# Kernel optimization log

Hardware: AMD Instinct MI355X
Metric: run time of the kernel (lower is better)

## Reference

```python
import jax, jax.numpy as jnp
import numpy as np

B, P, N, C = 8, 4, 512, 768
H = 12
HD = C // H  # 64
SCALE = HD ** -0.5


def setup_inputs() -> dict:
    key = jax.random.key(0)
    k1, k2, k3 = jax.random.split(key, 3)
    x = jax.random.normal(k1, (B, P, N, C), dtype=jnp.float32)
    W_qkv = jax.random.normal(k2, (3 * C, C), dtype=jnp.float32) * (C ** -0.5)
    W_proj = jax.random.normal(k3, (C, C), dtype=jnp.float32) * (C ** -0.5)
    b_proj = jnp.zeros((C,), dtype=jnp.float32)
    return {"x": x, "W_qkv": W_qkv, "W_proj": W_proj, "b_proj": b_proj}


def reference(x, W_qkv, W_proj, b_proj):
    b, p, n, c = x.shape
    # qkv projection (no bias): (B,P,N,3C) -> (B,P,N,3,H,HD)
    qkv = jnp.einsum('bpnc,dc->bpnd', x, W_qkv).reshape(b, p, n, 3, H, HD)
    # -> (3, B, P, H, N, HD)
    qkv = jnp.transpose(qkv, (3, 0, 1, 4, 2, 5))
    q, k, v = qkv[0], qkv[1], qkv[2]
    # scaled dot-product attention per (batch, patch, head)
    attn = jnp.einsum('bphnd,bphmd->bphnm', q * SCALE, k)
    attn = jax.nn.softmax(attn, axis=-1)
    out = jnp.einsum('bphnm,bphmd->bphnd', attn, v)
    # merge heads: (B,P,N,H,HD) -> (B,P,N,C)
    out = jnp.transpose(out, (0, 1, 3, 2, 4)).reshape(b, p, n, c)
    return jnp.einsum('bpnc,dc->bpnd', out, W_proj) + b_proj
```

## Files before the change

### kernel.cpp

```cpp
#include <hip/hip_runtime.h>

typedef _Float16 f16x8 __attribute__((ext_vector_type(8)));
typedef _Float16 f16x4 __attribute__((ext_vector_type(4)));
typedef unsigned short u16x8 __attribute__((ext_vector_type(8)));
typedef unsigned short u16x4 __attribute__((ext_vector_type(4)));
typedef float f32x4 __attribute__((ext_vector_type(4)));

#define GLOAD_LDS16(GP, LP)                                                        \
  __builtin_amdgcn_global_load_lds((const __attribute__((address_space(1))) void*)(GP), \
                                   (__attribute__((address_space(3))) void*)(LP), 16, 0, 0)

__device__ __forceinline__ unsigned int pkh(float a, float b) {
  return __builtin_bit_cast(unsigned int, __builtin_amdgcn_cvt_pkrtz(a, b));
}
__device__ __forceinline__ f16x8 ldfragh(const unsigned short* p) {
  return __builtin_bit_cast(f16x8, *(const u16x8*)p);
}
__device__ __forceinline__ f16x4 ldfragh4(const unsigned short* p) {
  return __builtin_bit_cast(f16x4, *(const u16x4*)p);
}
__device__ __forceinline__ f32x4 mfma32h(f16x8 a, f16x8 b, f32x4 c) {
  return __builtin_amdgcn_mfma_f32_16x16x32_f16(a, b, c, 0, 0, 0);
}
__device__ __forceinline__ f32x4 mfma16h(f16x4 a, f16x4 b, f32x4 c) {
  return __builtin_amdgcn_mfma_f32_16x16x16f16(a, b, c, 0, 0, 0);
}

#define MTOK   16384
#define CDIM   768
#define C3     2304
#define C2     1536
#define NX     12582912
#define NQW    1769472
#define NPW    589824

#define QSCALE_LOG2E 0.1803368801111204f

#define XB_OFF    0ul
#define WQKV_OFF  25165824ul
#define WPROJ_OFF 28704768ul
#define QK_OFF    29884416ul
#define VT_OFF    80216064ul

__global__ __launch_bounds__(256) void convert_kernel(
    const float* __restrict__ x, const float* __restrict__ wqkv,
    const float* __restrict__ wproj, unsigned short* __restrict__ xb,
    unsigned short* __restrict__ wqkvb, unsigned short* __restrict__ wprojb) {
  const int NX4 = NX / 4, NQ4 = NQW / 4, NP4 = NPW / 4;
  const int total = NX4 + NQ4 + NP4;
  for (int i = blockIdx.x * 256 + threadIdx.x; i < total; i += gridDim.x * 256) {
    const float4* src; unsigned short* dst; float scale = 1.f; int j;
    if (i < NX4) { src = (const float4*)x; dst = xb; j = i; }
    else if (i < NX4 + NQ4) {
      j = i - NX4; src = (const float4*)wqkv; dst = wqkvb;
      int d = (j * 4) / CDIM; if (d < CDIM) scale = QSCALE_LOG2E;
    } else { j = i - NX4 - NQ4; src = (const float4*)wproj; dst = wprojb; }
    float4 v = src[j];
    uint2 pk; pk.x = pkh(v.x * scale, v.y * scale); pk.y = pkh(v.z * scale, v.w * scale);
    *(uint2*)(dst + (long)j * 4) = pk;
  }
}

template <int MODE>
__global__ __launch_bounds__(256) void gemm_bt(
    const unsigned short* __restrict__ A, const unsigned short* __restrict__ B,
    unsigned short* __restrict__ out_hf, float* __restrict__ out_f32,
    const float* __restrict__ bias) {
  constexpr int K = 768;
  constexpr bool SWAP = (MODE != 1);
  __shared__ unsigned short As[128 * 64];
  __shared__ unsigned short Bs[128 * 64];
  const int tid = threadIdx.x;
  const int wave = tid >> 6, lane = tid & 63;
  const int wy = wave >> 1, wx = wave & 1;
  const int l15 = lane & 15, quad = lane >> 4;
  const int bm = blockIdx.x, bn = blockIdx.y;

  f32x4 acc[4][4];
  for (int i = 0; i < 4; i++)
    for (int j = 0; j < 4; j++) acc[i][j] = f32x4{0.f, 0.f, 0.f, 0.f};

  const long Abase = (long)bm * 128 * K;
  const long Bbase = (long)bn * 128 * K;

  long goff[4]; int ldsoff[4];
  for (int i = 0; i < 4; i++) {
    int c = wave * 256 + i * 64 + lane;
    int row = c >> 3, q = c & 7;
    int srcq = q ^ (row & 7);
    goff[i] = (long)row * K + srcq * 8;
    ldsoff[i] = c * 8;
  }
  const int slot0 = (quad ^ (l15 & 7)) * 8;
  const int slot1 = ((4 + quad) ^ (l15 & 7)) * 8;

  for (int kk = 0; kk < K; kk += 64) {
    for (int i = 0; i < 4; i++) {
      GLOAD_LDS16(A + Abase + goff[i] + kk, As + ldsoff[i]);
      GLOAD_LDS16(B + Bbase + goff[i] + kk, Bs + ldsoff[i]);
    }
    __syncthreads();
    for (int ks = 0; ks < 2; ks++) {
      const int sl = ks ? slot1 : slot0;
      f16x8 af[4], bfr[4];
      for (int mt = 0; mt < 4; mt++) af[mt]  = ldfragh(As + (wy * 64 + mt * 16 + l15) * 64 + sl);
      for (int nt = 0; nt < 4; nt++) bfr[nt] = ldfragh(Bs + (wx * 64 + nt * 16 + l15) * 64 + sl);
      for (int mt = 0; mt < 4; mt++)
        for (int nt = 0; nt < 4; nt++) {
          if (SWAP) acc[mt][nt] = mfma32h(bfr[nt], af[mt], acc[mt][nt]);
          else      acc[mt][nt] = mfma32h(af[mt], bfr[nt], acc[mt][nt]);
        }
    }
    __syncthreads();
  }

  if (MODE == 0) {
    for (int mt = 0; mt < 4; mt++) {
      int m = bm * 128 + wy * 64 + mt * 16 + l15;
      for (int nt = 0; nt < 4; nt++) {
        int d0 = bn * 128 + wx * 64 + nt * 16 + quad * 4;
        uint2 pk; pk.x = pkh(acc[mt][nt][0], acc[mt][nt][1]);
        pk.y = pkh(acc[mt][nt][2], acc[mt][nt][3]);
        *(uint2*)(out_hf + (long)m * C2 + d0) = pk;
      }
    }
  } else if (MODE == 1) {
    for (int mt = 0; mt < 4; mt++) {
      int mg = bm * 128 + wy * 64 + mt * 16 + quad * 4;
      int bp = mg >> 9, n0 = mg & 511;
      for (int nt = 0; nt < 4; nt++) {
        int dp = bn * 128 + wx * 64 + nt * 16 + l15;
        int hh = dp >> 6, e = dp & 63;
        uint2 pk; pk.x = pkh(acc[mt][nt][0], acc[mt][nt][1]);
        pk.y = pkh(acc[mt][nt][2], acc[mt][nt][3]);
        *(uint2*)(out_hf + ((long)((bp * 12 + hh) * 64 + e) * 512 + n0)) = pk;
      }
    }
  } else {
    for (int nt = 0; nt < 4; nt++) {
      int d0 = bn * 128 + wx * 64 + nt * 16 + quad * 4;
      float4 bv = *(const float4*)(bias + d0);
      for (int mt = 0; mt < 4; mt++) {
        int m = bm * 128 + wy * 64 + mt * 16 + l15;
        float4 o;
        o.x = acc[mt][nt][0] + bv.x; o.y = acc[mt][nt][1] + bv.y;
        o.z = acc[mt][nt][2] + bv.z; o.w = acc[mt][nt][3] + bv.w;
        *(float4*)(out_f32 + (long)m * CDIM + d0) = o;
      }
    }
  }
}

__global__ __launch_bounds__(256, 4) void attn_kernel(
    const unsigned short* __restrict__ qk, const unsigned short* __restrict__ vT,
    unsigned short* __restrict__ aout) {
  const int bph = blockIdx.x;
  const int qt  = blockIdx.y;
  const int bp = bph / 12, h = bph % 12;
  const int tid = threadIdx.x;
  const int wave = tid >> 6, lane = tid & 63;
  const int l15 = lane & 15, quad = lane >> 4;

  __shared__ unsigned short Qs[128 * 72];
  __shared__ unsigned short Ks[64 * 72];
  __shared__ unsigned short Vs[64 * 72];

  const unsigned short* Qg = qk + (long)(bp * 512 + qt * 128) * C2 + h * 64;
  const unsigned short* Kg = qk + (long)(bp * 512) * C2 + CDIM + h * 64;
  const unsigned short* Vg = vT + (long)(bp * 12 + h) * 64 * 512;

  for (int i = 0; i < 4; i++) {
    int c = tid + i * 256;
    int row = c >> 3, c8 = c & 7;
    *(uint4*)(Qs + row * 72 + c8 * 8) = *(const uint4*)(Qg + (long)row * C2 + c8 * 8);
  }

  f32x4 o[2][4];
  float lrow[2] = {0.f, 0.f};
  for (int a = 0; a < 2; a++)
    for (int b = 0; b < 4; b++) o[a][b] = f32x4{0.f, 0.f, 0.f, 0.f};

  for (int ch = 0; ch < 8; ch++) {
    if (ch) __syncthreads();
    for (int i = 0; i < 2; i++) {
      int c = tid + i * 256;
      int row = c >> 3, c8 = c & 7;
      *(uint4*)(Ks + row * 72 + c8 * 8) = *(const uint4*)(Kg + (long)(ch * 64 + row) * C2 + c8 * 8);
      *(uint4*)(Vs + row * 72 + c8 * 8) = *(const uint4*)(Vg + (long)row * 512 + ch * 64 + c8 * 8);
    }
    __syncthreads();

    f32x4 st[2][4];
    for (int a = 0; a < 2; a++)
      for (int b = 0; b < 4; b++) st[a][b] = f32x4{0.f, 0.f, 0.f, 0.f};
    for (int ks = 0; ks < 2; ks++) {
      f16x8 qf[2];
      qf[0] = ldfragh(Qs + (wave * 32 +      l15) * 72 + ks * 32 + quad * 8);
      qf[1] = ldfragh(Qs + (wave * 32 + 16 + l15) * 72 + ks * 32 + quad * 8);
      for (int nt = 0; nt < 4; nt++) {
        f16x8 kf = ldfragh(Ks + (nt * 16 + l15) * 72 + ks * 32 + quad * 8);
        st[0][nt] = mfma32h(kf, qf[0], st[0][nt]);
        st[1][nt] = mfma32h(kf, qf[1], st[1][nt]);
      }
    }

    f16x4 pf[2][4];
    for (int mt2 = 0; mt2 < 2; mt2++) {
      float rs = 0.f;
      for (int nt = 0; nt < 4; nt++) {
        f32x4 p;
        for (int r = 0; r < 4; r++) {
          p[r] = __builtin_amdgcn_exp2f(st[mt2][nt][r]);
          rs += p[r];
        }
        uint2 pk2; pk2.x = pkh(p[0], p[1]); pk2.y = pkh(p[2], p[3]);
        pf[mt2][nt] = __builtin_bit_cast(f16x4, pk2);
      }
      lrow[mt2] += rs;
    }

    for (int nt = 0; nt < 4; nt++)
      for (int et = 0; et < 4; et++) {
        f16x4 vf = ldfragh4(Vs + (et * 16 + l15) * 72 + nt * 16 + quad * 4);
        o[0][et] = mfma16h(vf, pf[0][nt], o[0][et]);
        o[1][et] = mfma16h(vf, pf[1][nt], o[1][et]);
      }
  }

  for (int mt2 = 0; mt2 < 2; mt2++) {
    float l = lrow[mt2];
    l += __shfl_xor(l, 16);
    l += __shfl_xor(l, 32);
    float inv = 1.f / l;
    int q = qt * 128 + wave * 32 + mt2 * 16 + l15;
    for (int et = 0; et < 4; et++) {
      uint2 pk; pk.x = pkh(o[mt2][et][0] * inv, o[mt2][et][1] * inv);
      pk.y = pkh(o[mt2][et][2] * inv, o[mt2][et][3] * inv);
      *(uint2*)(aout + (long)(bp * 512 + q) * CDIM + h * 64 + et * 16 + quad * 4) = pk;
    }
  }
}

extern "C" void kernel_launch(void* const* d_in, const int* in_sizes, int n_in,
                              void* d_out, int out_size, void* d_ws, size_t ws_size,
                              hipStream_t stream) {
  (void)in_sizes; (void)n_in; (void)out_size; (void)ws_size;
  const float* x     = (const float*)d_in[0];
  const float* wqkv  = (const float*)d_in[1];
  const float* wproj = (const float*)d_in[2];
  const float* bproj = (const float*)d_in[3];
  float* out = (float*)d_out;
  char* ws = (char*)d_ws;

  unsigned short* xb     = (unsigned short*)(ws + XB_OFF);
  unsigned short* wqkvb  = (unsigned short*)(ws + WQKV_OFF);
  unsigned short* wprojb = (unsigned short*)(ws + WPROJ_OFF);
  unsigned short* qkbuf  = (unsigned short*)(ws + QK_OFF);
  unsigned short* vTbuf  = (unsigned short*)(ws + VT_OFF);
  unsigned short* attn_o = xb;

  convert_kernel<<<2048, 256, 0, stream>>>(x, wqkv, wproj, xb, wqkvb, wprojb);
  gemm_bt<0><<<dim3(128, 12), 256, 0, stream>>>(xb, wqkvb, qkbuf, nullptr, nullptr);
  gemm_bt<1><<<dim3(128, 6), 256, 0, stream>>>(xb, wqkvb + (long)C2 * CDIM, vTbuf, nullptr, nullptr);
  attn_kernel<<<dim3(384, 4), 256, 0, stream>>>(qkbuf, vTbuf, attn_o);
  gemm_bt<2><<<dim3(128, 6), 256, 0, stream>>>(attn_o, wprojb, nullptr, out, bproj);
}
```

Before: 262.3 us.

## Merge QK and V projection GEMMs and register-prefetch tiles instead of LDS-direct loads

The separate QK and V projection launches become one launch over an 18-column grid. Blocks with bn<12 write the row-major QK buffer, and the rest write the transposed V buffer, using a runtime swap flag to pick the MFMA operand order. The direct global-to-LDS loads are replaced by a register prefetch: the next K-slice is loaded into registers while MFMAs run on the current LDS tile. This removes one launch and its tail and overlaps global latency with compute, but costs more registers, adds an extra store pass through VGPRs, and makes the MFMA operand order a runtime branch.

```diff
diff --git a/kernel.cpp b/kernel.cpp
--- a/kernel.cpp
+++ b/kernel.cpp
@@ -5,10 +5,6 @@
 typedef unsigned short u16x8 __attribute__((ext_vector_type(8)));
 typedef unsigned short u16x4 __attribute__((ext_vector_type(4)));
 typedef float f32x4 __attribute__((ext_vector_type(4)));
-
-#define GLOAD_LDS16(GP, LP)                                                        \
-  __builtin_amdgcn_global_load_lds((const __attribute__((address_space(1))) void*)(GP), \
-                                   (__attribute__((address_space(3))) void*)(LP), 16, 0, 0)
 
 __device__ __forceinline__ unsigned int pkh(float a, float b) {
   return __builtin_bit_cast(unsigned int, __builtin_amdgcn_cvt_pkrtz(a, b));
@@ -64,10 +60,9 @@
 template <int MODE>
 __global__ __launch_bounds__(256) void gemm_bt(
     const unsigned short* __restrict__ A, const unsigned short* __restrict__ B,
-    unsigned short* __restrict__ out_hf, float* __restrict__ out_f32,
-    const float* __restrict__ bias) {
+    unsigned short* __restrict__ out_hf, unsigned short* __restrict__ out_vT,
+    float* __restrict__ out_f32, const float* __restrict__ bias) {
   constexpr int K = 768;
-  constexpr bool SWAP = (MODE != 1);
   __shared__ unsigned short As[128 * 64];
   __shared__ unsigned short Bs[128 * 64];
   const int tid = threadIdx.x;
@@ -75,13 +70,14 @@
   const int wy = wave >> 1, wx = wave & 1;
   const int l15 = lane & 15, quad = lane >> 4;
   const int bm = blockIdx.x, bn = blockIdx.y;
+  const bool swap = (MODE == 2) || (bn < 12);
 
   f32x4 acc[4][4];
   for (int i = 0; i < 4; i++)
     for (int j = 0; j < 4; j++) acc[i][j] = f32x4{0.f, 0.f, 0.f, 0.f};
 
-  const long Abase = (long)bm * 128 * K;
-  const long Bbase = (long)bn * 128 * K;
+  const unsigned short* Ab = A + (long)bm * 128 * K;
+  const unsigned short* Bb = B + (long)bn * 128 * K;
 
   long goff[4]; int ldsoff[4];
   for (int i = 0; i < 4; i++) {
@@ -94,12 +90,24 @@
   const int slot0 = (quad ^ (l15 & 7)) * 8;
   const int slot1 = ((4 + quad) ^ (l15 & 7)) * 8;
 
+  uint4 pA[4], pB[4];
+  for (int i = 0; i < 4; i++) {
+    pA[i] = *(const uint4*)(Ab + goff[i]);
+    pB[i] = *(const uint4*)(Bb + goff[i]);
+  }
+
   for (int kk = 0; kk < K; kk += 64) {
     for (int i = 0; i < 4; i++) {
-      GLOAD_LDS16(A + Abase + goff[i] + kk, As + ldsoff[i]);
-      GLOAD_LDS16(B + Bbase + goff[i] + kk, Bs + ldsoff[i]);
+      *(uint4*)(As + ldsoff[i]) = pA[i];
+      *(uint4*)(Bs + ldsoff[i]) = pB[i];
     }
     __syncthreads();
+    if (kk + 64 < K) {
+      for (int i = 0; i < 4; i++) {
+        pA[i] = *(const uint4*)(Ab + goff[i] + kk + 64);
+        pB[i] = *(const uint4*)(Bb + goff[i] + kk + 64);
+      }
+    }
     for (int ks = 0; ks < 2; ks++) {
       const int sl = ks ? slot1 : slot0;
       f16x8 af[4], bfr[4];
@@ -107,7 +115,7 @@
       for (int nt = 0; nt < 4; nt++) bfr[nt] = ldfragh(Bs + (wx * 64 + nt * 16 + l15) * 64 + sl);
       for (int mt = 0; mt < 4; mt++)
         for (int nt = 0; nt < 4; nt++) {
-          if (SWAP) acc[mt][nt] = mfma32h(bfr[nt], af[mt], acc[mt][nt]);
+          if (swap) acc[mt][nt] = mfma32h(bfr[nt], af[mt], acc[mt][nt]);
           else      acc[mt][nt] = mfma32h(af[mt], bfr[nt], acc[mt][nt]);
         }
     }
@@ -115,25 +123,27 @@
   }
 
   if (MODE == 0) {
-    for (int mt = 0; mt < 4; mt++) {
-      int m = bm * 128 + wy * 64 + mt * 16 + l15;
-      for (int nt = 0; nt < 4; nt++) {
-        int d0 = bn * 128 + wx * 64 + nt * 16 + quad * 4;
-        uint2 pk; pk.x = pkh(acc[mt][nt][0], acc[mt][nt][1]);
-        pk.y = pkh(acc[mt][nt][2], acc[mt][nt][3]);
-        *(uint2*)(out_hf + (long)m * C2 + d0) = pk;
-      }
-    }
-  } else if (MODE == 1) {
-    for (int mt = 0; mt < 4; mt++) {
-      int mg = bm * 128 + wy * 64 + mt * 16 + quad * 4;
-      int bp = mg >> 9, n0 = mg & 511;
-      for (int nt = 0; nt < 4; nt++) {
-        int dp = bn * 128 + wx * 64 + nt * 16 + l15;
-        int hh = dp >> 6, e = dp & 63;
-        uint2 pk; pk.x = pkh(acc[mt][nt][0], acc[mt][nt][1]);
-        pk.y = pkh(acc[mt][nt][2], acc[mt][nt][3]);
-        *(uint2*)(out_hf + ((long)((bp * 12 + hh) * 64 + e) * 512 + n0)) = pk;
+    if (bn < 12) {
+      for (int mt = 0; mt < 4; mt++) {
+        int m = bm * 128 + wy * 64 + mt * 16 + l15;
+        for (int nt = 0; nt < 4; nt++) {
+          int d0 = bn * 128 + wx * 64 + nt * 16 + quad * 4;
+          uint2 pk; pk.x = pkh(acc[mt][nt][0], acc[mt][nt][1]);
+          pk.y = pkh(acc[mt][nt][2], acc[mt][nt][3]);
+          *(uint2*)(out_hf + (long)m * C2 + d0) = pk;
+        }
+      }
+    } else {
+      for (int mt = 0; mt < 4; mt++) {
+        int mg = bm * 128 + wy * 64 + mt * 16 + quad * 4;
+        int bp = mg >> 9, n0 = mg & 511;
+        for (int nt = 0; nt < 4; nt++) {
+          int dp = bn * 128 - C2 + wx * 64 + nt * 16 + l15;
+          int hh = dp >> 6, e = dp & 63;
+          uint2 pk; pk.x = pkh(acc[mt][nt][0], acc[mt][nt][1]);
+          pk.y = pkh(acc[mt][nt][2], acc[mt][nt][3]);
+          *(uint2*)(out_vT + ((long)((bp * 12 + hh) * 64 + e) * 512 + n0)) = pk;
+        }
       }
     }
   } else {
@@ -260,8 +270,7 @@
   unsigned short* attn_o = xb;
 
   convert_kernel<<<2048, 256, 0, stream>>>(x, wqkv, wproj, xb, wqkvb, wprojb);
-  gemm_bt<0><<<dim3(128, 12), 256, 0, stream>>>(xb, wqkvb, qkbuf, nullptr, nullptr);
-  gemm_bt<1><<<dim3(128, 6), 256, 0, stream>>>(xb, wqkvb + (long)C2 * CDIM, vTbuf, nullptr, nullptr);
+  gemm_bt<0><<<dim3(128, 18), 256, 0, stream>>>(xb, wqkvb, qkbuf, vTbuf, nullptr, nullptr);
   attn_kernel<<<dim3(384, 4), 256, 0, stream>>>(qkbuf, vTbuf, attn_o);
-  gemm_bt<2><<<dim3(128, 6), 256, 0, stream>>>(attn_o, wprojb, nullptr, out, bproj);
-}
+  gemm_bt<2><<<dim3(128, 6), 256, 0, stream>>>(attn_o, wprojb, nullptr, nullptr, out, bproj);
+}
```

After: 507.9 us. +93.6%, slower.
